# Kernel tuning notes

Hardware: AMD Instinct MI355X
Metric: run time of the kernel (lower is better)

## Reference

```python
import jax, jax.numpy as jnp
import numpy as np


def setup_inputs() -> dict:
    key = jax.random.key(0)
    ks = jax.random.split(key, 6)
    B, S, F, U = 64, 1024, 1024, 1024
    scale = 0.02
    return {
        "features": jax.random.normal(ks[0], (B, S, F), dtype=jnp.float32),
        "hidden": jax.random.normal(ks[1], (B, U), dtype=jnp.float32),
        "W1_w": jax.random.normal(ks[2], (F, U), dtype=jnp.float32) * scale,
        "W1_b": jnp.zeros((U,), dtype=jnp.float32),
        "W2_w": jax.random.normal(ks[3], (U, U), dtype=jnp.float32) * scale,
        "W2_b": jnp.zeros((U,), dtype=jnp.float32),
        "V_w": jax.random.normal(ks[4], (U, 1), dtype=jnp.float32) * scale,
        "V_b": jnp.zeros((1,), dtype=jnp.float32),
    }


def reference(features, hidden, W1_w, W1_b, W2_w, W2_b, V_w, V_b):
    # features: [B, S, F]; hidden: [B, H]
    # score = tanh(W1(features) + W2(hidden)[:, None, :])  -> [B, S, U]
    proj_f = jnp.einsum("bsf,fu->bsu", features, W1_w) + W1_b
    proj_h = hidden @ W2_w + W2_b  # [B, U]
    score = jnp.tanh(proj_f + proj_h[:, None, :])
    # logits: [B, S, 1]; softmax over seq axis (axis=1)
    logits = jnp.einsum("bsu,uo->bso", score, V_w) + V_b
    attention_weights = jax.nn.softmax(logits, axis=1)
    # context: sum over seq of weights * features -> [B, F]
    context_vector = jnp.sum(attention_weights * features, axis=1)
    return context_vector, attention_weights
```

## Files before the change

### kernel.cpp

```cpp
#include <hip/hip_runtime.h>
#include <hip/hip_bf16.h>
#include <stdint.h>

#define B_ 64
#define S_ 1024
#define F_ 1024
#define U_ 1024

typedef __attribute__((ext_vector_type(4))) float  f4;
typedef __attribute__((ext_vector_type(4))) float  f32x4;
typedef __attribute__((ext_vector_type(8))) short  short8;
typedef __attribute__((ext_vector_type(4))) short  bf16x4;
typedef unsigned int u32;

static __device__ __forceinline__ short f2bf(float x){
    union { float f; uint32_t u; } v; v.f = x;
    uint32_t u = v.u;
    u += 0x7fffu + ((u >> 16) & 1u);
    return (short)(u >> 16);
}

static __device__ __forceinline__ void glds16(const void* g, void* l){
    __builtin_amdgcn_global_load_lds(
        (const __attribute__((address_space(1))) u32*)g,
        (__attribute__((address_space(3))) u32*)l, 16, 0, 0);
}

static __device__ __forceinline__ float fast_tanh(float x){
    float e = __expf(2.f * x);
    return 1.f - 2.f / (e + 1.f);
}

__global__ void pack_w1(const float* __restrict__ W1, short* __restrict__ Bws){
    int g = blockIdx.x * 256 + threadIdx.x;
    int n    =  g        & 127;
    int kgrp = (g >> 7)  & 3;
    int nb   = (g >> 9)  & 7;
    int kb   =  g >> 12;
    int u  = nb*128 + n;
    int f0 = kb*32 + kgrp*8;
    short8 o;
#pragma unroll
    for (int j = 0; j < 8; ++j)
        o[j] = f2bf(W1[(size_t)(f0 + j)*U_ + u]);
    *(short8*)&Bws[(size_t)g * 8] = o;
}

__global__ __launch_bounds__(256) void pack_feat(const float* __restrict__ F,
                                                 short* __restrict__ out){
    __shared__ short tile[4096];
    const int mb = blockIdx.x >> 5, kt = blockIdx.x & 31;
    const int t = threadIdx.x;
    const float* base = F + (size_t)mb*128*1024 + kt*32;
#pragma unroll
    for (int i = 0; i < 4; ++i){
        int li = i*256 + t;
        int row = li >> 3, c4 = li & 7;
        f4 v = *(const f4*)(base + (size_t)row*1024 + c4*4);
        bf16x4 s;
        s[0]=f2bf(v[0]); s[1]=f2bf(v[1]); s[2]=f2bf(v[2]); s[3]=f2bf(v[3]);
        int kgrp = c4 >> 1, half = c4 & 1;
        *(bf16x4*)&tile[(kgrp*128 + row)*8 + half*4] = s;
    }
    __syncthreads();
    short8* dst = (short8*)&out[(size_t)blockIdx.x * 4096];
#pragma unroll
    for (int i = 0; i < 2; ++i){
        int e = i*256 + t;
        dst[e] = *(const short8*)&tile[e*8];
    }
}

__global__ void hb_kernel(const float* __restrict__ hidden, const float* __restrict__ W2,
                          const float* __restrict__ W2b, const float* __restrict__ W1b,
                          float* __restrict__ hb){
    __shared__ float hs[4][256];
    const int ub = blockIdx.x, kc = blockIdx.y, bg = blockIdx.z, t = threadIdx.x;
    for (int i = t; i < 1024; i += 256)
        hs[i>>8][i&255] = hidden[(size_t)(bg*4 + (i>>8))*1024 + kc*256 + (i&255)];
    __syncthreads();
    const int u = ub*256 + t;
    const float* w2 = W2 + (size_t)(kc*256)*1024 + u;
    float a0=0.f, a1=0.f, a2=0.f, a3=0.f;
#pragma unroll 4
    for (int k = 0; k < 256; ++k){
        float w = w2[(size_t)k*1024];
        a0 = fmaf(hs[0][k], w, a0);
        a1 = fmaf(hs[1][k], w, a1);
        a2 = fmaf(hs[2][k], w, a2);
        a3 = fmaf(hs[3][k], w, a3);
    }
    float base = (kc == 0) ? (W1b[u] + W2b[u]) : 0.f;
    atomicAdd(&hb[(size_t)(bg*4+0)*1024 + u], base + a0);
    atomicAdd(&hb[(size_t)(bg*4+1)*1024 + u], base + a1);
    atomicAdd(&hb[(size_t)(bg*4+2)*1024 + u], base + a2);
    atomicAdd(&hb[(size_t)(bg*4+3)*1024 + u], base + a3);
}

static __device__ __forceinline__ void swz_mbnb(int bid, int& mb, int& nb){
    int xcd = bid & 7;
    int seq = bid >> 3;
    nb = seq & 7;
    mb = xcd*64 + (seq >> 3);
}

__global__ __launch_bounds__(256) void gemm_v2(
        const short* __restrict__ Abf, const short* __restrict__ Bws,
        const float* __restrict__ hb, const float* __restrict__ Vw,
        float* __restrict__ logits){
    __shared__ short Ab0[4096], Ab1[4096];
    __shared__ short Bb0[4096], Bb1[4096];

    const int t = threadIdx.x;
    int mb, nb; swz_mbnb(blockIdx.x, mb, nb);
    const int m0 = mb*128, n0 = nb*128;
    const int batch = m0 >> 10;
    const int w = t >> 6, l = t & 63;
    const int wr = w >> 1, wc = w & 1;
    const int kg = l >> 4, fr = l & 15;

    const char* Asrc = (const char*)Abf + ((size_t)(mb*32) << 13) + (w<<11) + (l<<4);
    const char* Bsrc = (const char*)Bws + ((size_t)nb << 13) + (w<<11) + (l<<4);
    char* Adst0 = (char*)Ab0 + (w<<11);  char* Adst1 = (char*)Ab1 + (w<<11);
    char* Bdst0 = (char*)Bb0 + (w<<11);  char* Bdst1 = (char*)Bb1 + (w<<11);

#define STAGE(D, kt) do{                                     \
        const char* as_ = Asrc + ((size_t)(kt) << 13);       \
        const char* bs_ = Bsrc + ((size_t)(kt) << 16);       \
        glds16(as_,        Adst##D);                         \
        glds16(as_ + 1024, Adst##D + 1024);                  \
        glds16(bs_,        Bdst##D);                         \
        glds16(bs_ + 1024, Bdst##D + 1024);                  \
    }while(0)

#define COMPUTE(AB, BB) do{                                                   \
        short8 af[4], bfr[4];                                                 \
        _Pragma("unroll")                                                     \
        for (int i = 0; i < 4; ++i)                                           \
            af[i] = *(const short8*)&AB[(kg*128 + wr*64 + i*16 + fr)*8];      \
        _Pragma("unroll")                                                     \
        for (int j = 0; j < 4; ++j)                                           \
            bfr[j] = *(const short8*)&BB[(kg*128 + wc*64 + j*16 + fr)*8];     \
        _Pragma("unroll")                                                     \
        for (int i = 0; i < 4; ++i)                                           \
            _Pragma("unroll")                                                 \
            for (int j = 0; j < 4; ++j)                                       \
                acc[i][j] = __builtin_amdgcn_mfma_f32_16x16x32_bf16(          \
                                af[i], bfr[j], acc[i][j], 0, 0, 0);           \
    }while(0)

    f32x4 acc[4][4];
#pragma unroll
    for (int i = 0; i < 4; ++i)
#pragma unroll
        for (int j = 0; j < 4; ++j) acc[i][j] = (f32x4)0.f;

    STAGE(0, 0);
    asm volatile("s_waitcnt vmcnt(0)");
    __syncthreads();

    for (int kt = 0; kt < 32; kt += 2){
        STAGE(1, kt + 1);
        COMPUTE(Ab0, Bb0);
        __syncthreads();
        if (kt + 2 < 32) STAGE(0, kt + 2);
        COMPUTE(Ab1, Bb1);
        __syncthreads();
    }
#undef STAGE
#undef COMPUTE

    float hv[4], vv[4];
#pragma unroll
    for (int j = 0; j < 4; ++j){
        int u = n0 + wc*64 + j*16 + fr;
        hv[j] = hb[batch*U_ + u];
        vv[j] = Vw[u];
    }
#pragma unroll
    for (int i = 0; i < 4; ++i){
#pragma unroll
        for (int reg = 0; reg < 4; ++reg){
            float sum = 0.f;
#pragma unroll
            for (int j = 0; j < 4; ++j){
                float sc = fast_tanh(acc[i][j][reg] + hv[j]);
                sum = fmaf(vv[j], sc, sum);
            }
            sum += __shfl_xor(sum, 1, 64);
            sum += __shfl_xor(sum, 2, 64);
            sum += __shfl_xor(sum, 4, 64);
            sum += __shfl_xor(sum, 8, 64);
            if (fr == 0)
                atomicAdd(&logits[m0 + wr*64 + i*16 + kg*4 + reg], sum);
        }
    }
}

__global__ __launch_bounds__(256) void gemm_fb(
        const float* __restrict__ A, const short* __restrict__ Bws,
        const float* __restrict__ hb, const float* __restrict__ Vw,
        float* __restrict__ logits){
    __shared__ short Abuf[4096];
    __shared__ short Bbuf[2][4096];

    const int t = threadIdx.x;
    int mb, nb; swz_mbnb(blockIdx.x, mb, nb);
    const int m0 = mb*128, n0 = nb*128;
    const int batch = m0 >> 10;
    const int w = t >> 6, l = t & 63;
    const int wr = w >> 1, wc = w & 1;
    const int kg = l >> 4, fr = l & 15;
    const int ar = t >> 1, ah = t & 1;

    const float* aptr = A + (size_t)(m0 + ar)*F_ + ah*16;

    f32x4 acc[4][4];
#pragma unroll
    for (int i = 0; i < 4; ++i)
#pragma unroll
        for (int j = 0; j < 4; ++j) acc[i][j] = (f32x4)0.f;

    f4 a0 = *(const f4*)(aptr + 0);
    f4 a1 = *(const f4*)(aptr + 4);
    f4 a2 = *(const f4*)(aptr + 8);
    f4 a3 = *(const f4*)(aptr + 12);
    {
        const char* src = (const char*)Bws + ((size_t)nb << 13) + (w<<11) + (l<<4);
        char* dst = (char*)&Bbuf[0][0] + (w<<11);
        glds16(src, dst);
        glds16(src + 1024, dst + 1024);
    }

    for (int kt = 0; kt < 32; ++kt){
        const int sel = kt & 1;
        short8 s0, s1;
        s0[0]=f2bf(a0[0]); s0[1]=f2bf(a0[1]); s0[2]=f2bf(a0[2]); s0[3]=f2bf(a0[3]);
        s0[4]=f2bf(a1[0]); s0[5]=f2bf(a1[1]); s0[6]=f2bf(a1[2]); s0[7]=f2bf(a1[3]);
        s1[0]=f2bf(a2[0]); s1[1]=f2bf(a2[1]); s1[2]=f2bf(a2[2]); s1[3]=f2bf(a2[3]);
        s1[4]=f2bf(a3[0]); s1[5]=f2bf(a3[1]); s1[6]=f2bf(a3[2]); s1[7]=f2bf(a3[3]);
        *(short8*)&Abuf[((2*ah+0)*128 + ar)*8] = s0;
        *(short8*)&Abuf[((2*ah+1)*128 + ar)*8] = s1;
        __syncthreads();

        if (kt < 31){
            const float* ap = aptr + (kt+1)*32;
            a0 = *(const f4*)(ap + 0);
            a1 = *(const f4*)(ap + 4);
            a2 = *(const f4*)(ap + 8);
            a3 = *(const f4*)(ap + 12);
            const char* src = (const char*)Bws + ((size_t)((kt+1)*8 + nb) << 13) + (w<<11) + (l<<4);
            char* dst = (char*)&Bbuf[sel^1][0] + (w<<11);
            glds16(src, dst);
            glds16(src + 1024, dst + 1024);
        }

        short8 af[4], bfr[4];
#pragma unroll
        for (int i = 0; i < 4; ++i)
            af[i] = *(const short8*)&Abuf[(kg*128 + wr*64 + i*16 + fr)*8];
#pragma unroll
        for (int j = 0; j < 4; ++j)
            bfr[j] = *(const short8*)&Bbuf[sel][(kg*128 + wc*64 + j*16 + fr)*8];
#pragma unroll
        for (int i = 0; i < 4; ++i)
#pragma unroll
            for (int j = 0; j < 4; ++j)
                acc[i][j] = __builtin_amdgcn_mfma_f32_16x16x32_bf16(af[i], bfr[j], acc[i][j], 0, 0, 0);
        __syncthreads();
    }

    float hv[4], vv[4];
#pragma unroll
    for (int j = 0; j < 4; ++j){
        int u = n0 + wc*64 + j*16 + fr;
        hv[j] = hb[batch*U_ + u];
        vv[j] = Vw[u];
    }
#pragma unroll
    for (int i = 0; i < 4; ++i){
#pragma unroll
        for (int reg = 0; reg < 4; ++reg){
            float sum = 0.f;
#pragma unroll
            for (int j = 0; j < 4; ++j){
                float sc = fast_tanh(acc[i][j][reg] + hv[j]);
                sum = fmaf(vv[j], sc, sum);
            }
            sum += __shfl_xor(sum, 1, 64);
            sum += __shfl_xor(sum, 2, 64);
            sum += __shfl_xor(sum, 4, 64);
            sum += __shfl_xor(sum, 8, 64);
            if (fr == 0)
                atomicAdd(&logits[m0 + wr*64 + i*16 + kg*4 + reg], sum);
        }
    }
}

__global__ void softmax_seq(float* __restrict__ lg){
    __shared__ float red[4], red2[4];
    int b = blockIdx.x, t = threadIdx.x;
    float v[4];
#pragma unroll
    for (int c = 0; c < 4; ++c) v[c] = lg[b*1024 + c*256 + t];
    float mx = fmaxf(fmaxf(v[0], v[1]), fmaxf(v[2], v[3]));
#pragma unroll
    for (int off = 32; off >= 1; off >>= 1) mx = fmaxf(mx, __shfl_xor(mx, off, 64));
    if ((t & 63) == 0) red[t >> 6] = mx;
    __syncthreads();
    mx = fmaxf(fmaxf(red[0], red[1]), fmaxf(red[2], red[3]));
    float e[4], s = 0.f;
#pragma unroll
    for (int c = 0; c < 4; ++c){ e[c] = __expf(v[c] - mx); s += e[c]; }
#pragma unroll
    for (int off = 32; off >= 1; off >>= 1) s += __shfl_xor(s, off, 64);
    if ((t & 63) == 0) red2[t >> 6] = s;
    __syncthreads();
    s = red2[0] + red2[1] + red2[2] + red2[3];
    float inv = 1.f / s;
#pragma unroll
    for (int c = 0; c < 4; ++c) lg[b*1024 + c*256 + t] = e[c] * inv;
}

__global__ void context_kernel(const float* __restrict__ feats, const float* __restrict__ wts,
                               float* __restrict__ ctx){
    __shared__ float wsh[128];
    int sh = blockIdx.x, b = blockIdx.y, t = threadIdx.x;
    if (t < 128) wsh[t] = wts[b*1024 + sh*128 + t];
    __syncthreads();
    const f4* fp = (const f4*)(feats + ((size_t)b*1024 + sh*128)*1024) + t;
    f4 a0 = (f4)0.f, a1 = (f4)0.f, a2 = (f4)0.f, a3 = (f4)0.f;
    for (int s = 0; s < 128; s += 4){
        a0 += wsh[s+0] * fp[(size_t)(s+0)*256];
        a1 += wsh[s+1] * fp[(size_t)(s+1)*256];
        a2 += wsh[s+2] * fp[(size_t)(s+2)*256];
        a3 += wsh[s+3] * fp[(size_t)(s+3)*256];
    }
    f4 r = (a0 + a1) + (a2 + a3);
    float* c = ctx + b*1024 + t*4;
    atomicAdd(c+0, r[0]); atomicAdd(c+1, r[1]);
    atomicAdd(c+2, r[2]); atomicAdd(c+3, r[3]);
}

extern "C" void kernel_launch(void* const* d_in, const int* in_sizes, int n_in,
                              void* d_out, int out_size, void* d_ws, size_t ws_size,
                              hipStream_t stream){
    const float* features = (const float*)d_in[0];
    const float* hidden   = (const float*)d_in[1];
    const float* W1w      = (const float*)d_in[2];
    const float* W1b      = (const float*)d_in[3];
    const float* W2w      = (const float*)d_in[4];
    const float* W2b      = (const float*)d_in[5];
    const float* Vw       = (const float*)d_in[6];

    float* out = (float*)d_out;
    float* ctx = out;
    float* att = out + 65536;

    short* Bws    = (short*)d_ws;
    float* hb     = (float*)((char*)d_ws + (size_t)2*1024*1024);
    short* featbf = (short*)((char*)d_ws + (size_t)2*1024*1024 + 256*1024);

    const size_t need = (size_t)2*1024*1024 + 256*1024 + (size_t)128*1024*1024;

    (void)hipMemsetAsync(d_out, 0, (size_t)131072 * sizeof(float), stream);
    (void)hipMemsetAsync(hb, 0, (size_t)65536 * sizeof(float), stream);
    pack_w1<<<512, 256, 0, stream>>>(W1w, Bws);
    hb_kernel<<<dim3(4, 4, 16), 256, 0, stream>>>(hidden, W2w, W2b, W1b, hb);

    if (ws_size >= need){
        pack_feat<<<16384, 256, 0, stream>>>(features, featbf);
        gemm_v2<<<4096, 256, 0, stream>>>(featbf, Bws, hb, Vw, att);
    } else {
        gemm_fb<<<4096, 256, 0, stream>>>(features, Bws, hb, Vw, att);
    }

    softmax_seq<<<64, 256, 0, stream>>>(att);
    context_kernel<<<dim3(8, 64), 256, 0, stream>>>(features, att, ctx);
}
```

Measured before the change: 674.7 us.

## Enlarge GEMM M-tile to 256 rows and restructure context reduction

The main bf16 GEMM now has each block compute a 256x128 tile instead of 128x128, with 8x4 MFMA accumulators per wave, so each staged B tile is reused across twice as many rows and half as many blocks launch. The fallback GEMM keeps the old swizzle via a separate helper. The context kernel now covers the whole sequence per block for a 128-column slice, reducing partials in shared memory and storing directly, which removes the atomics and the memset of the context output. The larger tile doubles accumulator registers and LDS use, which may lower occupancy.

```diff
diff --git a/kernel.cpp b/kernel.cpp
--- a/kernel.cpp
+++ b/kernel.cpp
@@ -101,57 +101,58 @@
     int xcd = bid & 7;
     int seq = bid >> 3;
     nb = seq & 7;
-    mb = xcd*64 + (seq >> 3);
+    mb = xcd*32 + (seq >> 3);
 }
 
 __global__ __launch_bounds__(256) void gemm_v2(
         const short* __restrict__ Abf, const short* __restrict__ Bws,
         const float* __restrict__ hb, const float* __restrict__ Vw,
         float* __restrict__ logits){
-    __shared__ short Ab0[4096], Ab1[4096];
+    __shared__ short Ab0[8192], Ab1[8192];
     __shared__ short Bb0[4096], Bb1[4096];
 
     const int t = threadIdx.x;
     int mb, nb; swz_mbnb(blockIdx.x, mb, nb);
-    const int m0 = mb*128, n0 = nb*128;
+    const int m0 = mb*256, n0 = nb*128;
     const int batch = m0 >> 10;
     const int w = t >> 6, l = t & 63;
     const int wr = w >> 1, wc = w & 1;
     const int kg = l >> 4, fr = l & 15;
 
-    const char* Asrc = (const char*)Abf + ((size_t)(mb*32) << 13) + (w<<11) + (l<<4);
-    const char* Bsrc = (const char*)Bws + ((size_t)nb << 13) + (w<<11) + (l<<4);
-    char* Adst0 = (char*)Ab0 + (w<<11);  char* Adst1 = (char*)Ab1 + (w<<11);
-    char* Bdst0 = (char*)Bb0 + (w<<11);  char* Bdst1 = (char*)Bb1 + (w<<11);
-
-#define STAGE(D, kt) do{                                     \
-        const char* as_ = Asrc + ((size_t)(kt) << 13);       \
-        const char* bs_ = Bsrc + ((size_t)(kt) << 16);       \
-        glds16(as_,        Adst##D);                         \
-        glds16(as_ + 1024, Adst##D + 1024);                  \
-        glds16(bs_,        Bdst##D);                         \
-        glds16(bs_ + 1024, Bdst##D + 1024);                  \
+    const char* AsrcA = (const char*)Abf + ((size_t)mb << 19) + (l<<4);
+    const char* BsrcB = (const char*)Bws + ((size_t)nb << 13) + (l<<4);
+
+#define STAGE(D, kt) do{                                                      \
+        const char* a0_ = AsrcA + ((size_t)(kt) << 13);                       \
+        const char* a1_ = a0_ + (32 << 13);             \
+        const char* bs_ = BsrcB + ((size_t)(kt) << 16);                       \
+        glds16(a0_ + (w<<10),       (char*)Ab##D + (w<<10));                  \
+        glds16(a0_ + ((4+w)<<10),   (char*)Ab##D + ((4+w)<<10));              \
+        glds16(a1_ + (w<<10),       (char*)Ab##D + ((8+w)<<10));              \
+        glds16(a1_ + ((4+w)<<10),   (char*)Ab##D + ((12+w)<<10));             \
+        glds16(bs_ + (w<<10),       (char*)Bb##D + (w<<10));                  \
+        glds16(bs_ + ((4+w)<<10),   (char*)Bb##D + ((4+w)<<10));              \
     }while(0)
 
 #define COMPUTE(AB, BB) do{                                                   \
-        short8 af[4], bfr[4];                                                 \
-        _Pragma("unroll")                                                     \
-        for (int i = 0; i < 4; ++i)                                           \
-            af[i] = *(const short8*)&AB[(kg*128 + wr*64 + i*16 + fr)*8];      \
+        short8 af[8], bfr[4];                                                 \
         _Pragma("unroll")                                                     \
         for (int j = 0; j < 4; ++j)                                           \
             bfr[j] = *(const short8*)&BB[(kg*128 + wc*64 + j*16 + fr)*8];     \
         _Pragma("unroll")                                                     \
-        for (int i = 0; i < 4; ++i)                                           \
+        for (int i = 0; i < 8; ++i)                                           \
+            af[i] = *(const short8*)&AB[wr*4096 + (kg*128 + i*16 + fr)*8];    \
+        _Pragma("unroll")                                                     \
+        for (int i = 0; i < 8; ++i)                                           \
             _Pragma("unroll")                                                 \
             for (int j = 0; j < 4; ++j)                                       \
                 acc[i][j] = __builtin_amdgcn_mfma_f32_16x16x32_bf16(          \
                                 af[i], bfr[j], acc[i][j], 0, 0, 0);           \
     }while(0)
 
-    f32x4 acc[4][4];
-#pragma unroll
-    for (int i = 0; i < 4; ++i)
+    f32x4 acc[8][4];
+#pragma unroll
+    for (int i = 0; i < 8; ++i)
 #pragma unroll
         for (int j = 0; j < 4; ++j) acc[i][j] = (f32x4)0.f;
 
@@ -169,6 +170,113 @@
     }
 #undef STAGE
 #undef COMPUTE
+
+    float hv[4], vv[4];
+#pragma unroll
+    for (int j = 0; j < 4; ++j){
+        int u = n0 + wc*64 + j*16 + fr;
+        hv[j] = hb[batch*U_ + u];
+        vv[j] = Vw[u];
+    }
+#pragma unroll
+    for (int i = 0; i < 8; ++i){
+#pragma unroll
+        for (int reg = 0; reg < 4; ++reg){
+            float sum = 0.f;
+#pragma unroll
+            for (int j = 0; j < 4; ++j){
+                float sc = fast_tanh(acc[i][j][reg] + hv[j]);
+                sum = fmaf(vv[j], sc, sum);
+            }
+            sum += __shfl_xor(sum, 1, 64);
+            sum += __shfl_xor(sum, 2, 64);
+            sum += __shfl_xor(sum, 4, 64);
+            sum += __shfl_xor(sum, 8, 64);
+            if (fr == 0)
+                atomicAdd(&logits[m0 + wr*128 + i*16 + kg*4 + reg], sum);
+        }
+    }
+}
+
+static __device__ __forceinline__ void swz_mbnb_fb(int bid, int& mb, int& nb){
+    int xcd = bid & 7;
+    int seq = bid >> 3;
+    nb = seq & 7;
+    mb = xcd*64 + (seq >> 3);
+}
+
+__global__ __launch_bounds__(256) void gemm_fb(
+        const float* __restrict__ A, const short* __restrict__ Bws,
+        const float* __restrict__ hb, const float* __restrict__ Vw,
+        float* __restrict__ logits){
+    __shared__ short Abuf[4096];
+    __shared__ short Bbuf[2][4096];
+
+    const int t = threadIdx.x;
+    int mb, nb; swz_mbnb_fb(blockIdx.x, mb, nb);
+    const int m0 = mb*128, n0 = nb*128;
+    const int batch = m0 >> 10;
+    const int w = t >> 6, l = t & 63;
+    const int wr = w >> 1, wc = w & 1;
+    const int kg = l >> 4, fr = l & 15;
+    const int ar = t >> 1, ah = t & 1;
+
+    const float* aptr = A + (size_t)(m0 + ar)*F_ + ah*16;
+
+    f32x4 acc[4][4];
+#pragma unroll
+    for (int i = 0; i < 4; ++i)
+#pragma unroll
+        for (int j = 0; j < 4; ++j) acc[i][j] = (f32x4)0.f;
+
+    f4 a0 = *(const f4*)(aptr + 0);
+    f4 a1 = *(const f4*)(aptr + 4);
+    f4 a2 = *(const f4*)(aptr + 8);
+    f4 a3 = *(const f4*)(aptr + 12);
+    {
+        const char* src = (const char*)Bws + ((size_t)nb << 13) + (w<<11) + (l<<4);
+        char* dst = (char*)&Bbuf[0][0] + (w<<11);
+        glds16(src, dst);
+        glds16(src + 1024, dst + 1024);
+    }
+
+    for (int kt = 0; kt < 32; ++kt){
+        const int sel = kt & 1;
+        short8 s0, s1;
+        s0[0]=f2bf(a0[0]); s0[1]=f2bf(a0[1]); s0[2]=f2bf(a0[2]); s0[3]=f2bf(a0[3]);
+        s0[4]=f2bf(a1[0]); s0[5]=f2bf(a1[1]); s0[6]=f2bf(a1[2]); s0[7]=f2bf(a1[3]);
+        s1[0]=f2bf(a2[0]); s1[1]=f2bf(a2[1]); s1[2]=f2bf(a2[2]); s1[3]=f2bf(a2[3]);
+        s1[4]=f2bf(a3[0]); s1[5]=f2bf(a3[1]); s1[6]=f2bf(a3[2]); s1[7]=f2bf(a3[3]);
+        *(short8*)&Abuf[((2*ah+0)*128 + ar)*8] = s0;
+        *(short8*)&Abuf[((2*ah+1)*128 + ar)*8] = s1;
+        __syncthreads();
+
+        if (kt < 31){
+            const float* ap = aptr + (kt+1)*32;
+            a0 = *(const f4*)(ap + 0);
+            a1 = *(const f4*)(ap + 4);
+            a2 = *(const f4*)(ap + 8);
+            a3 = *(const f4*)(ap + 12);
+            const char* src = (const char*)Bws + ((size_t)((kt+1)*8 + nb) << 13) + (w<<11) + (l<<4);
+            char* dst = (char*)&Bbuf[sel^1][0] + (w<<11);
+            glds16(src, dst);
+            glds16(src + 1024, dst + 1024);
+        }
+
+        short8 af[4], bfr[4];
+#pragma unroll
+        for (int i = 0; i < 4; ++i)
+            af[i] = *(const short8*)&Abuf[(kg*128 + wr*64 + i*16 + fr)*8];
+#pragma unroll
+        for (int j = 0; j < 4; ++j)
+            bfr[j] = *(const short8*)&Bbuf[sel][(kg*128 + wc*64 + j*16 + fr)*8];
+#pragma unroll
+        for (int i = 0; i < 4; ++i)
+#pragma unroll
+            for (int j = 0; j < 4; ++j)
+                acc[i][j] = __builtin_amdgcn_mfma_f32_16x16x32_bf16(af[i], bfr[j], acc[i][j], 0, 0, 0);
+        __syncthreads();
+    }
 
     float hv[4], vv[4];
 #pragma unroll
@@ -197,106 +305,6 @@
     }
 }
 
-__global__ __launch_bounds__(256) void gemm_fb(
-        const float* __restrict__ A, const short* __restrict__ Bws,
-        const float* __restrict__ hb, const float* __restrict__ Vw,
-        float* __restrict__ logits){
-    __shared__ short Abuf[4096];
-    __shared__ short Bbuf[2][4096];
-
-    const int t = threadIdx.x;
-    int mb, nb; swz_mbnb(blockIdx.x, mb, nb);
-    const int m0 = mb*128, n0 = nb*128;
-    const int batch = m0 >> 10;
-    const int w = t >> 6, l = t & 63;
-    const int wr = w >> 1, wc = w & 1;
-    const int kg = l >> 4, fr = l & 15;
-    const int ar = t >> 1, ah = t & 1;
-
-    const float* aptr = A + (size_t)(m0 + ar)*F_ + ah*16;
-
-    f32x4 acc[4][4];
-#pragma unroll
-    for (int i = 0; i < 4; ++i)
-#pragma unroll
-        for (int j = 0; j < 4; ++j) acc[i][j] = (f32x4)0.f;
-
-    f4 a0 = *(const f4*)(aptr + 0);
-    f4 a1 = *(const f4*)(aptr + 4);
-    f4 a2 = *(const f4*)(aptr + 8);
-    f4 a3 = *(const f4*)(aptr + 12);
-    {
-        const char* src = (const char*)Bws + ((size_t)nb << 13) + (w<<11) + (l<<4);
-        char* dst = (char*)&Bbuf[0][0] + (w<<11);
-        glds16(src, dst);
-        glds16(src + 1024, dst + 1024);
-    }
-
-    for (int kt = 0; kt < 32; ++kt){
-        const int sel = kt & 1;
-        short8 s0, s1;
-        s0[0]=f2bf(a0[0]); s0[1]=f2bf(a0[1]); s0[2]=f2bf(a0[2]); s0[3]=f2bf(a0[3]);
-        s0[4]=f2bf(a1[0]); s0[5]=f2bf(a1[1]); s0[6]=f2bf(a1[2]); s0[7]=f2bf(a1[3]);
-        s1[0]=f2bf(a2[0]); s1[1]=f2bf(a2[1]); s1[2]=f2bf(a2[2]); s1[3]=f2bf(a2[3]);
-        s1[4]=f2bf(a3[0]); s1[5]=f2bf(a3[1]); s1[6]=f2bf(a3[2]); s1[7]=f2bf(a3[3]);
-        *(short8*)&Abuf[((2*ah+0)*128 + ar)*8] = s0;
-        *(short8*)&Abuf[((2*ah+1)*128 + ar)*8] = s1;
-        __syncthreads();
-
-        if (kt < 31){
-            const float* ap = aptr + (kt+1)*32;
-            a0 = *(const f4*)(ap + 0);
-            a1 = *(const f4*)(ap + 4);
-            a2 = *(const f4*)(ap + 8);
-            a3 = *(const f4*)(ap + 12);
-            const char* src = (const char*)Bws + ((size_t)((kt+1)*8 + nb) << 13) + (w<<11) + (l<<4);
-            char* dst = (char*)&Bbuf[sel^1][0] + (w<<11);
-            glds16(src, dst);
-            glds16(src + 1024, dst + 1024);
-        }
-
-        short8 af[4], bfr[4];
-#pragma unroll
-        for (int i = 0; i < 4; ++i)
-            af[i] = *(const short8*)&Abuf[(kg*128 + wr*64 + i*16 + fr)*8];
-#pragma unroll
-        for (int j = 0; j < 4; ++j)
-            bfr[j] = *(const short8*)&Bbuf[sel][(kg*128 + wc*64 + j*16 + fr)*8];
-#pragma unroll
-        for (int i = 0; i < 4; ++i)
-#pragma unroll
-            for (int j = 0; j < 4; ++j)
-                acc[i][j] = __builtin_amdgcn_mfma_f32_16x16x32_bf16(af[i], bfr[j], acc[i][j], 0, 0, 0);
-        __syncthreads();
-    }
-
-    float hv[4], vv[4];
-#pragma unroll
-    for (int j = 0; j < 4; ++j){
-        int u = n0 + wc*64 + j*16 + fr;
-        hv[j] = hb[batch*U_ + u];
-        vv[j] = Vw[u];
-    }
-#pragma unroll
-    for (int i = 0; i < 4; ++i){
-#pragma unroll
-        for (int reg = 0; reg < 4; ++reg){
-            float sum = 0.f;
-#pragma unroll
-            for (int j = 0; j < 4; ++j){
-                float sc = fast_tanh(acc[i][j][reg] + hv[j]);
-                sum = fmaf(vv[j], sc, sum);
-            }
-            sum += __shfl_xor(sum, 1, 64);
-            sum += __shfl_xor(sum, 2, 64);
-            sum += __shfl_xor(sum, 4, 64);
-            sum += __shfl_xor(sum, 8, 64);
-            if (fr == 0)
-                atomicAdd(&logits[m0 + wr*64 + i*16 + kg*4 + reg], sum);
-        }
-    }
-}
-
 __global__ void softmax_seq(float* __restrict__ lg){
     __shared__ float red[4], red2[4];
     int b = blockIdx.x, t = threadIdx.x;
@@ -322,24 +330,32 @@
     for (int c = 0; c < 4; ++c) lg[b*1024 + c*256 + t] = e[c] * inv;
 }
 
-__global__ void context_kernel(const float* __restrict__ feats, const float* __restrict__ wts,
-                               float* __restrict__ ctx){
-    __shared__ float wsh[128];
-    int sh = blockIdx.x, b = blockIdx.y, t = threadIdx.x;
-    if (t < 128) wsh[t] = wts[b*1024 + sh*128 + t];
-    __syncthreads();
-    const f4* fp = (const f4*)(feats + ((size_t)b*1024 + sh*128)*1024) + t;
-    f4 a0 = (f4)0.f, a1 = (f4)0.f, a2 = (f4)0.f, a3 = (f4)0.f;
-    for (int s = 0; s < 128; s += 4){
-        a0 += wsh[s+0] * fp[(size_t)(s+0)*256];
-        a1 += wsh[s+1] * fp[(size_t)(s+1)*256];
-        a2 += wsh[s+2] * fp[(size_t)(s+2)*256];
-        a3 += wsh[s+3] * fp[(size_t)(s+3)*256];
-    }
-    f4 r = (a0 + a1) + (a2 + a3);
-    float* c = ctx + b*1024 + t*4;
-    atomicAdd(c+0, r[0]); atomicAdd(c+1, r[1]);
-    atomicAdd(c+2, r[2]); atomicAdd(c+3, r[3]);
+__global__ __launch_bounds__(256) void context_kernel(const float* __restrict__ feats,
+                                                      const float* __restrict__ wts,
+                                                      float* __restrict__ ctx){
+    __shared__ float wsh[1024];
+    __shared__ f4 part[256];
+    const int fq = blockIdx.x, b = blockIdx.y, t = threadIdx.x;
+    for (int i = t; i < 1024; i += 256) wsh[i] = wts[b*1024 + i];
+    __syncthreads();
+    const int c  = fq*32 + (t & 31);
+    const int sr = t >> 5;
+    const f4* fp = (const f4*)(feats + (size_t)b*1024*1024) + c;
+    f4 a0=(f4)0.f, a1=(f4)0.f, a2=(f4)0.f, a3=(f4)0.f;
+    for (int s = sr; s < 1024; s += 32){
+        a0 += wsh[s]      * fp[(size_t)(s)     *256];
+        a1 += wsh[s +  8] * fp[(size_t)(s +  8)*256];
+        a2 += wsh[s + 16] * fp[(size_t)(s + 16)*256];
+        a3 += wsh[s + 24] * fp[(size_t)(s + 24)*256];
+    }
+    part[t] = (a0 + a1) + (a2 + a3);
+    __syncthreads();
+    if (t < 32){
+        f4 s = part[t];
+#pragma unroll
+        for (int r = 1; r < 8; ++r) s += part[t + r*32];
+        *(f4*)&ctx[b*1024 + fq*128 + t*4] = s;
+    }
 }
 
 extern "C" void kernel_launch(void* const* d_in, const int* in_sizes, int n_in,
@@ -363,14 +379,14 @@
 
     const size_t need = (size_t)2*1024*1024 + 256*1024 + (size_t)128*1024*1024;
 
-    (void)hipMemsetAsync(d_out, 0, (size_t)131072 * sizeof(float), stream);
+    (void)hipMemsetAsync(att, 0, (size_t)65536 * sizeof(float), stream);
     (void)hipMemsetAsync(hb, 0, (size_t)65536 * sizeof(float), stream);
     pack_w1<<<512, 256, 0, stream>>>(W1w, Bws);
     hb_kernel<<<dim3(4, 4, 16), 256, 0, stream>>>(hidden, W2w, W2b, W1b, hb);
 
     if (ws_size >= need){
         pack_feat<<<16384, 256, 0, stream>>>(features, featbf);
-        gemm_v2<<<4096, 256, 0, stream>>>(featbf, Bws, hb, Vw, att);
+        gemm_v2<<<2048, 256, 0, stream>>>(featbf, Bws, hb, Vw, att);
     } else {
         gemm_fb<<<4096, 256, 0, stream>>>(features, Bws, hb, Vw, att);
     }
```

Result: slower. 800.7 us (+18.7%).
